# Performance work log

Hardware: AMD Instinct MI355X
Metric: run time of the kernel (lower is better)

## Reference

```python
import jax, jax.numpy as jnp
import numpy as np
from jax import lax

G, CPG, KS, N = 8, 8, 3, 9  # groups, channels per group, kernel size, ks*ks


def conv2d(x, w, b=None, pad=1):
    y = lax.conv_general_dilated(x, w, (1, 1), [(pad, pad), (pad, pad)],
                                 dimension_numbers=('NCHW', 'OIHW', 'NCHW'))
    if b is not None:
        y = y + b[None, :, None, None]
    return y


def deform_group(x, f, pw, pb, mw, mb, cw):
    # x: sampled feature (anchor slice), f: offset source (motion slice); both (b,c,h,w)
    b, c, h, w = x.shape
    offset = conv2d(f, pw, pb)                      # (b, 2N, h, w)
    m = jax.nn.sigmoid(conv2d(f, mw, mb))           # (b, N, h, w) modulation
    off = jnp.transpose(offset, (0, 2, 3, 1))       # (b, h, w, 2N): first N rows(x), last N cols(y)
    rng = jnp.arange(-1, 2, dtype=x.dtype)
    pn_x = jnp.repeat(rng, KS)                      # kernel row offset, n = kr*3 + kc
    pn_y = jnp.tile(rng, KS)                        # kernel col offset
    p0_x = jnp.arange(1, h + 1, dtype=x.dtype)[:, None, None]  # base grid starts at 1 (padding=0 here)
    p0_y = jnp.arange(1, w + 1, dtype=x.dtype)[None, :, None]
    px = p0_x + pn_x + off[..., :N]                 # (b, h, w, N)
    py = p0_y + pn_y + off[..., N:]
    fx = jnp.floor(lax.stop_gradient(px))           # p.detach().floor() in the original
    fy = jnp.floor(lax.stop_gradient(py))
    qx_lt = jnp.clip(fx, 0, h - 1)
    qx_rb = jnp.clip(fx + 1, 0, h - 1)
    qy_lt = jnp.clip(fy, 0, w - 1)
    qy_rb = jnp.clip(fy + 1, 0, w - 1)
    px = jnp.clip(px, 0, h - 1)
    py = jnp.clip(py, 0, w - 1)
    g_lt = (1 + (qx_lt - px)) * (1 + (qy_lt - py))
    g_rb = (1 - (qx_rb - px)) * (1 - (qy_rb - py))
    g_lb = (1 + (qx_lt - px)) * (1 - (qy_rb - py))
    g_rt = (1 - (qx_rb - px)) * (1 + (qy_lt - py))
    x_flat = x.reshape(b, c, h * w)

    def gather(ix, iy):
        idx = (ix * w + iy).astype(jnp.int32).reshape(b, 1, -1)  # (b,1,h*w*N)
        return jnp.take_along_axis(x_flat, idx, axis=2).reshape(b, c, h, w, N)

    x_off = (g_lt[:, None] * gather(qx_lt, qy_lt) + g_rb[:, None] * gather(qx_rb, qy_rb)
             + g_lb[:, None] * gather(qx_lt, qy_rb) + g_rt[:, None] * gather(qx_rb, qy_lt))
    x_off = x_off * jnp.transpose(m, (0, 2, 3, 1))[:, None]      # apply modulation mask
    # fused equivalent of reshape to (b,c,h*3,w*3) + conv(k=3, stride=3, no bias)
    return jnp.einsum('bchwn,ocn->bohw', x_off, cw.reshape(cw.shape[0], c, N))


def reference(o, anchor, pw, pb, mw, mb, cw, w1, b1, w2, b2):
    b, C, h, w = anchor.shape
    xg = anchor.reshape(b, G, CPG, h, w).transpose(1, 0, 2, 3, 4)  # (G,b,c,h,w)
    fg = o.reshape(b, G, CPG, h, w).transpose(1, 0, 2, 3, 4)
    tg = jax.vmap(deform_group)(xg, fg, pw, pb, mw, mb, cw)        # (G,b,c,h,w)
    target = tg.transpose(1, 0, 2, 3, 4).reshape(b, C, h, w)
    target_ = jnp.concatenate([target, anchor], axis=1)            # (b,128,h,w)
    return target + conv2d(conv2d(target_, w1, b1), w2, b2)


def setup_inputs() -> dict:
    key = jax.random.key(0)
    ks = jax.random.split(key, 11)
    B, C, H, W = 4, 64, 128, 128
    return {
        'o': jax.random.normal(ks[0], (B, C, H, W), jnp.float32),
        'anchor': jax.random.normal(ks[1], (B, C, H, W), jnp.float32),
        'pw': jax.random.normal(ks[2], (G, 2 * N, CPG, 3, 3), jnp.float32) * 0.05,
        'pb': jax.random.normal(ks[3], (G, 2 * N), jnp.float32) * 0.05,
        'mw': jax.random.normal(ks[4], (G, N, CPG, 3, 3), jnp.float32) * 0.05,
        'mb': jax.random.normal(ks[5], (G, N), jnp.float32) * 0.05,
        'cw': jax.random.normal(ks[6], (G, CPG, CPG, 3, 3), jnp.float32) * 0.05,
        'w1': jax.random.normal(ks[7], (64, 128, 3, 3), jnp.float32) * 0.05,
        'b1': jax.random.normal(ks[8], (64,), jnp.float32) * 0.05,
        'w2': jax.random.normal(ks[9], (64, 64, 3, 3), jnp.float32) * 0.05,
        'b2': jax.random.normal(ks[10], (64,), jnp.float32) * 0.05,
    }
```

## Files before the change

### kernel.cpp

```cpp
#include <hip/hip_runtime.h>


typedef __attribute__((ext_vector_type(8))) short short8;
typedef __attribute__((ext_vector_type(4))) float float4v;
typedef __attribute__((ext_vector_type(2))) float float2v;

#define MFMA_B16(a, b, c) __builtin_amdgcn_mfma_f32_16x16x32_bf16(a, b, c, 0, 0, 0)

__device__ __forceinline__ ushort f2bf(float f) {
    union { float f; unsigned u; } v; v.f = f;
    unsigned r = v.u + 0x7FFFu + ((v.u >> 16) & 1u);
    return (ushort)(r >> 16);
}
__device__ __forceinline__ float bf2f(ushort h) {
    union { unsigned u; float f; } v; v.u = ((unsigned)h) << 16;
    return v.f;
}

__device__ __forceinline__ void tap_wo(int gy, int gx, int n,
                                       float ox, float oy, float mzv,
                                       float* W, int* O)
{
    int ky = n / 3, kx = n - ky * 3;
    float pxf = (float)(gy + ky) + ox;
    float pyf = (float)(gx + kx) + oy;
    float fx = floorf(pxf), fy = floorf(pyf);
    float qxl = fminf(fmaxf(fx, 0.f), 127.f);
    float qxr = fminf(fmaxf(fx + 1.f, 0.f), 127.f);
    float qyl = fminf(fmaxf(fy, 0.f), 127.f);
    float qyr = fminf(fmaxf(fy + 1.f, 0.f), 127.f);
    float pxc = fminf(fmaxf(pxf, 0.f), 127.f);
    float pyc = fminf(fmaxf(pyf, 0.f), 127.f);
    float glx = 1.f + (qxl - pxc), grx = 1.f - (qxr - pxc);
    float gly = 1.f + (qyl - pyc), gry = 1.f - (qyr - pyc);
    float mm = 1.f / (1.f + __expf(-mzv));
    W[0] = glx * gly * mm; W[1] = grx * gry * mm;
    W[2] = glx * gry * mm; W[3] = grx * gly * mm;
    int ixl = (int)qxl, ixr = (int)qxr, iyl = (int)qyl, iyr = (int)qyr;
    O[0] = ixl * 128 + iyl; O[1] = ixr * 128 + iyr;
    O[2] = ixl * 128 + iyr; O[3] = ixr * 128 + iyl;
}

__device__ __forceinline__ short8 interp4(const float* W, const short8* cv)
{
    union U { short8 s; uint4 u; };
    uint4 c[4];
    #pragma unroll
    for (int j = 0; j < 4; ++j) { U t; t.s = cv[j]; c[j] = t.u; }
    U out;
    #pragma unroll
    for (int p = 0; p < 4; ++p) {
        float2v acc = {0.f, 0.f};
        #pragma unroll
        for (int j = 0; j < 4; ++j) {
            unsigned d = (&c[j].x)[p];
            float2v cc = {__uint_as_float(d << 16),
                          __uint_as_float(d & 0xffff0000u)};
            float2v Wv = {W[j], W[j]};
            acc = __builtin_elementwise_fma(cc, Wv, acc);
        }
        unsigned u0 = __float_as_uint(acc.x), u1 = __float_as_uint(acc.y);
        (&out.u.x)[p] = __builtin_amdgcn_perm(u1, u0, 0x07060302u);
    }
    return out.s;
}

__global__ __launch_bounds__(256) void prep(
    const float* __restrict__ anchor,
    const float* __restrict__ w1, const float* __restrict__ w2,
    const float* __restrict__ pw, const float* __restrict__ pb,
    const float* __restrict__ mw, const float* __restrict__ mb,
    const float* __restrict__ cw,
    ushort* __restrict__ anc_g,
    ushort* __restrict__ rw1, ushort* __restrict__ rw2,
    ushort* __restrict__ rpwh, ushort* __restrict__ rpwl,
    ushort* __restrict__ rcw)
{
    const int blk = blockIdx.x;
    if (blk < 256) {
        int pix = (blk & 63) * 256 + threadIdx.x;
        int b = blk >> 6;
        ushort tmp[64];
        #pragma unroll
        for (int ch = 0; ch < 64; ++ch)
            tmp[ch] = f2bf(anchor[(((size_t)(b * 64 + ch)) << 14) + pix]);
        #pragma unroll
        for (int grp = 0; grp < 8; ++grp) {
            short8 v;
            #pragma unroll
            for (int j = 0; j < 8; ++j) v[j] = (short)tmp[grp * 8 + j];
            *(short8*)(anc_g + ((size_t)(b * 8 + grp)) * 131072 + (size_t)pix * 8) = v;
        }
        return;
    }
    int i = (blk - 256) * 256 + threadIdx.x;
    if (i < 73728) {
        int kk = i & 31, r = i >> 5, oc = r & 63, r2 = r >> 6;
        int ks = r2 & 3, s = r2 >> 2, ic = ks * 32 + kk;
        rw1[i] = f2bf(w1[(oc * 128 + ic) * 9 + s]);
    }
    if (i < 36864) {
        int kk = i & 31, r = i >> 5, oc = r & 63, r2 = r >> 6;
        int ks = r2 & 1, s = r2 >> 1, ic = ks * 32 + kk;
        rw2[i] = f2bf(w2[(oc * 64 + ic) * 9 + s]);
    }
    if (i < 24576) {
        int kk = i & 31, r = i >> 5, n = r & 31, r2 = r >> 5;
        int ks = r2 % 3, g = r2 / 3, k = ks * 32 + kk;
        float v = 0.f;
        if (k < 72) {
            int s = k >> 3, ic = k & 7;
            if (n < 18)      v = pw[((g * 18 + n) * 8 + ic) * 9 + s];
            else if (n < 27) v = mw[((g * 9 + (n - 18)) * 8 + ic) * 9 + s];
        } else if (k == 72) {
            if (n < 18)      v = pb[g * 18 + n];
            else if (n < 27) v = mb[g * 9 + (n - 18)];
        }
        ushort h = f2bf(v);
        rpwh[i] = h;
        rpwl[i] = f2bf(v - bf2f(h));
    }
    if (i < 12288) {
        int kk = i & 31, r = i >> 5, oc = r & 15, r2 = r >> 4;
        int ks = r2 % 3, g = r2 / 3, k = ks * 32 + kk;
        float v = 0.f;
        if (k < 72 && oc < 8) {
            int n = k >> 3, ic = k & 7;
            v = cw[((g * 8 + oc) * 8 + ic) * 9 + n];
        }
        rcw[i] = f2bf(v);
    }
}

__global__ __launch_bounds__(256, 4) void deform_mfma(
    const float* __restrict__ o, const ushort* __restrict__ anc_g,
    const ushort* __restrict__ rpwh, const ushort* __restrict__ rpwl,
    const ushort* __restrict__ rcw,
    ushort* __restrict__ xcat_g)
{
    const int tile = blockIdx.x, g = blockIdx.y, b = blockIdx.z;
    const int ty0 = (tile >> 3) * 16, tx0 = (tile & 7) * 16;
    const int tid = threadIdx.x, lane = tid & 63, wave = tid >> 6;
    const int l15 = lane & 15, quad = lane >> 4;

    __shared__ __align__(16) ushort sU[19008];
    ushort* slabh = sU;
    ushort* slabl = sU + 2592;
    float*  sOff  = (float*)((char*)sU + 10368);
    ushort* sEu   = sU;

    const float* obase = o + (((size_t)(b * 64 + g * 8)) << 14);
    #pragma unroll
    for (int pass = 0; pass < 2; ++pass) {
        int pix = tid + pass * 256;
        if (pix < 324) {
            int r = pix / 18, c = pix - r * 18;
            int gy = ty0 + r - 1, gx = tx0 + c - 1;
            short8 vh = {0, 0, 0, 0, 0, 0, 0, 0};
            short8 vl = {0, 0, 0, 0, 0, 0, 0, 0};
            if ((unsigned)gy < 128u && (unsigned)gx < 128u) {
                const float* p0 = obase + (gy << 7) + gx;
                #pragma unroll
                for (int ic = 0; ic < 8; ++ic) {
                    float v = p0[(size_t)ic << 14];
                    ushort h = f2bf(v);
                    vh[ic] = (short)h;
                    vl[ic] = (short)f2bf(v - bf2f(h));
                }
            }
            *(short8*)(&slabh[pix * 8]) = vh;
            *(short8*)(&slabl[pix * 8]) = vl;
        }
    }
    __syncthreads();

    float4v offacc[4][2] = {};
    #pragma unroll
    for (int ks = 0; ks < 3; ++ks) {
        short8 Bh[2], Bl[2];
        #pragma unroll
        for (int nf = 0; nf < 2; ++nf) {
            int off = ((g * 3 + ks) * 32 + nf * 16 + l15) * 32 + quad * 8;
            Bh[nf] = *(const short8*)(rpwh + off);
            Bl[nf] = *(const short8*)(rpwl + off);
        }
        short8 Ah[4], Al[4];
        if (ks < 2) {
            int s = ks * 4 + quad, sy = s / 3, sx = s - sy * 3;
            #pragma unroll
            for (int py = 0; py < 4; ++py) {
                int row = wave * 4 + py;
                int sl = ((row + sy) * 18 + l15 + sx) * 8;
                Ah[py] = *(const short8*)(&slabh[sl]);
                Al[py] = *(const short8*)(&slabl[sl]);
            }
        } else {
            #pragma unroll
            for (int py = 0; py < 4; ++py) {
                short8 zh = {0, 0, 0, 0, 0, 0, 0, 0};
                short8 zl = {0, 0, 0, 0, 0, 0, 0, 0};
                if (quad == 0) {
                    int row = wave * 4 + py;
                    int sl = ((row + 2) * 18 + l15 + 2) * 8;
                    zh = *(const short8*)(&slabh[sl]);
                    zl = *(const short8*)(&slabl[sl]);
                } else if (quad == 1) {
                    zh[0] = (short)0x3F80;
                }
                Ah[py] = zh; Al[py] = zl;
            }
        }
        #pragma unroll
        for (int py = 0; py < 4; ++py)
            #pragma unroll
            for (int nf = 0; nf < 2; ++nf) {
                offacc[py][nf] = MFMA_B16(Ah[py], Bh[nf], offacc[py][nf]);
                offacc[py][nf] = MFMA_B16(Ah[py], Bl[nf], offacc[py][nf]);
                offacc[py][nf] = MFMA_B16(Al[py], Bh[nf], offacc[py][nf]);
            }
    }
    #pragma unroll
    for (int py = 0; py < 4; ++py) {
        int p0 = (wave * 4 + py) * 16 + quad * 4;
        #pragma unroll
        for (int nf = 0; nf < 2; ++nf) {
            int ch = nf * 16 + l15;
            if (ch < 27) {
                #pragma unroll
                for (int reg = 0; reg < 4; ++reg)
                    sOff[(p0 + reg) * 27 + ch] = offacc[py][nf][reg];
            }
        }
    }

    short8 Bw[3];
    #pragma unroll
    for (int ks = 0; ks < 3; ++ks)
        Bw[ks] = *(const short8*)(rcw + (((g * 3 + ks) * 16 + l15) * 32 + quad * 8));

    const ushort* gb = anc_g + ((size_t)(b * 8 + g)) * 131072;
    const int n1 = quad, n2 = quad + 4;
    float4v cacc[4] = {};
    #pragma unroll
    for (int py = 0; py < 4; ++py) {
        int prow = wave * 4 + py;
        int p = prow * 16 + l15;
        int gy = ty0 + prow, gx = tx0 + l15;

        float W[8]; int O[8];
        tap_wo(gy, gx, n1, sOff[p * 27 + n1], sOff[p * 27 + 9 + n1],
               sOff[p * 27 + 18 + n1], &W[0], &O[0]);
        tap_wo(gy, gx, n2, sOff[p * 27 + n2], sOff[p * 27 + 9 + n2],
               sOff[p * 27 + 18 + n2], &W[4], &O[4]);
        short8 cv[8];
        #pragma unroll
        for (int j = 0; j < 8; ++j)
            cv[j] = *(const short8*)(gb + (size_t)O[j] * 8);
        short8 A0 = interp4(&W[0], &cv[0]);
        short8 A1 = interp4(&W[4], &cv[4]);
        short8 A2 = {0, 0, 0, 0, 0, 0, 0, 0};
        if (quad == 0) {
            float W2[4]; int O2[4];
            tap_wo(gy, gx, 8, sOff[p * 27 + 8], sOff[p * 27 + 17],
                   sOff[p * 27 + 26], W2, O2);
            short8 c2[4];
            #pragma unroll
            for (int j = 0; j < 4; ++j)
                c2[j] = *(const short8*)(gb + (size_t)O2[j] * 8);
            A2 = interp4(W2, c2);
        }
        cacc[py] = MFMA_B16(A0, Bw[0], cacc[py]);
        cacc[py] = MFMA_B16(A1, Bw[1], cacc[py]);
        cacc[py] = MFMA_B16(A2, Bw[2], cacc[py]);
    }

    __syncthreads();
    #pragma unroll
    for (int py = 0; py < 4; ++py) {
        if (l15 < 8) {
            #pragma unroll
            for (int reg = 0; reg < 4; ++reg)
                sEu[((wave * 4 + py) * 16 + quad * 4 + reg) * 8 + l15] =
                    f2bf(cacc[py][reg]);
        }
    }
    __syncthreads();
    {
        const int gy = ty0 + (tid >> 4), gx = tx0 + (tid & 15);
        short8 pk = *(const short8*)(&sEu[tid * 8]);
        *(short8*)(xcat_g + ((size_t)(b * 8 + g)) * 131072
                   + (size_t)((gy << 7) + gx) * 8) = pk;
    }
}

__global__ __launch_bounds__(256, 4) void conv1_mfma(
    const ushort* __restrict__ xg, const ushort* __restrict__ ag,
    const ushort* __restrict__ rw1, const float* __restrict__ b1,
    ushort* __restrict__ t1)
{
    const int patch = blockIdx.x, b = blockIdx.y;
    const int px0 = (patch & 7) * 16, py0 = (patch >> 3) * 8;
    const int tid = threadIdx.x, lane = tid & 63, wave = tid >> 6;
    const int mhalf = wave & 1, nhalf = wave >> 1;
    const int l15 = lane & 15, quad = lane >> 4;

    __shared__ __align__(16) ushort sA[180 * 72];

    float4v acc[4][2] = {};
    #pragma unroll
    for (int ph = 0; ph < 2; ++ph) {
        if (ph) __syncthreads();
        const ushort* src = (ph == 0) ? xg : ag;
        for (int task = tid; task < 1440; task += 256) {
            int grp = task / 180, pix = task - grp * 180;
            int r = pix / 18, c = pix - r * 18;
            int gy = py0 + r - 1, gx = px0 + c - 1;
            short8 v = {0, 0, 0, 0, 0, 0, 0, 0};
            if ((unsigned)gy < 128u && (unsigned)gx < 128u) {
                const ushort* plane = src + ((size_t)(b * 8 + grp)) * 131072;
                v = *(const short8*)(plane + (size_t)((gy << 7) + gx) * 8);
            }
            *(short8*)(&sA[pix * 72 + grp * 8]) = v;
        }
        __syncthreads();

        #pragma unroll
        for (int ks2 = 0; ks2 < 2; ++ks2) {
            const int ks = ph * 2 + ks2;
            #pragma unroll
            for (int ky = 0; ky < 3; ++ky) {
                short8 Bf[3][2];
                #pragma unroll
                for (int kx = 0; kx < 3; ++kx)
                    #pragma unroll
                    for (int nf = 0; nf < 2; ++nf) {
                        int oc = nhalf * 32 + nf * 16 + l15;
                        Bf[kx][nf] = *(const short8*)(rw1 +
                            ((((ky * 3 + kx) * 4 + ks) * 64 + oc) * 32 + quad * 8));
                    }
                #pragma unroll
                for (int py = 0; py < 4; ++py) {
                    int slabrow = mhalf * 4 + py + ky;
                    #pragma unroll
                    for (int kx = 0; kx < 3; ++kx) {
                        short8 A = *(const short8*)(&sA[(slabrow * 18 + l15 + kx) * 72
                                                        + ks2 * 32 + quad * 8]);
                        #pragma unroll
                        for (int nf = 0; nf < 2; ++nf)
                            acc[py][nf] = MFMA_B16(A, Bf[kx][nf], acc[py][nf]);
                    }
                }
            }
        }
    }
    __syncthreads();
    ushort* sE = sA;
    #pragma unroll
    for (int nf = 0; nf < 2; ++nf) {
        int oc = nhalf * 32 + nf * 16 + l15;
        float bias = b1[oc];
        #pragma unroll
        for (int py = 0; py < 4; ++py) {
            int row = mhalf * 4 + py;
            #pragma unroll
            for (int reg = 0; reg < 4; ++reg)
                sE[(row * 16 + quad * 4 + reg) * 64 + oc] = f2bf(acc[py][nf][reg] + bias);
        }
    }
    __syncthreads();
    {
        const size_t nbase = ((size_t)b) << 20;
        int pix = tid >> 1, half = tid & 1;
        int gy = py0 + (pix >> 4), gx = px0 + (pix & 15);
        ushort* dst = t1 + nbase + (size_t)((gy << 7) + gx) * 64 + half * 32;
        const ushort* sp = sE + pix * 64 + half * 32;
        #pragma unroll
        for (int j = 0; j < 4; ++j)
            *(short8*)(dst + j * 8) = *(const short8*)(sp + j * 8);
    }
}

__global__ __launch_bounds__(256, 4) void conv2_mfma(
    const ushort* __restrict__ t1, const ushort* __restrict__ rw2,
    const float* __restrict__ b2, const ushort* __restrict__ xg,
    float* __restrict__ out)
{
    const int patch = blockIdx.x, b = blockIdx.y;
    const int px0 = (patch & 7) * 16, py0 = (patch >> 3) * 8;
    const int tid = threadIdx.x, lane = tid & 63, wave = tid >> 6;
    const int ohalf = wave & 1, rhalf = wave >> 1;
    const int l15 = lane & 15, quad = lane >> 4;

    __shared__ __align__(16) ushort sX[180 * 72];

    const size_t nbase = ((size_t)b) << 20;
    for (int task = tid; task < 1440; task += 256) {
        int pix = task >> 3, grp = task & 7;
        int r = pix / 18, c = pix - r * 18;
        int gy = py0 + r - 1, gx = px0 + c - 1;
        short8 v = {0, 0, 0, 0, 0, 0, 0, 0};
        if ((unsigned)gy < 128u && (unsigned)gx < 128u)
            v = *(const short8*)(t1 + nbase + (size_t)((gy << 7) + gx) * 64 + grp * 8);
        *(short8*)(&sX[pix * 72 + grp * 8]) = v;
    }
    __syncthreads();

    float4v acc[2][4] = {};
    #pragma unroll
    for (int ks = 0; ks < 2; ++ks) {
        #pragma unroll
        for (int ky = 0; ky < 3; ++ky) {
            short8 Aw[3][2];
            #pragma unroll
            for (int kx = 0; kx < 3; ++kx)
                #pragma unroll
                for (int mf = 0; mf < 2; ++mf) {
                    int oc = ohalf * 32 + mf * 16 + l15;
                    Aw[kx][mf] = *(const short8*)(rw2 +
                        ((((ky * 3 + kx) * 2 + ks) * 64 + oc) * 32 + quad * 8));
                }
            #pragma unroll
            for (int py = 0; py < 4; ++py) {
                int slabrow = rhalf * 4 + py + ky;
                #pragma unroll
                for (int kx = 0; kx < 3; ++kx) {
                    short8 Bx = *(const short8*)(&sX[(slabrow * 18 + l15 + kx) * 72
                                                     + ks * 32 + quad * 8]);
                    #pragma unroll
                    for (int mf = 0; mf < 2; ++mf)
                        acc[mf][py] = MFMA_B16(Aw[kx][mf], Bx, acc[mf][py]);
                }
            }
        }
    }
    #pragma unroll
    for (int mf = 0; mf < 2; ++mf)
        #pragma unroll
        for (int reg = 0; reg < 4; ++reg) {
            int oc = ohalf * 32 + mf * 16 + quad * 4 + reg;
            float bias = b2[oc];
            const ushort* rplane = xg + ((size_t)(b * 8 + (oc >> 3))) * 131072 + (oc & 7);
            #pragma unroll
            for (int py = 0; py < 4; ++py) {
                int gy = py0 + rhalf * 4 + py, gx = px0 + l15;
                int pix = (gy << 7) + gx;
                float res = bf2f(rplane[(size_t)pix * 8]);
                out[(((size_t)(b * 64 + oc)) << 14) + pix] = acc[mf][py][reg] + bias + res;
            }
        }
}

extern "C" void kernel_launch(void* const* d_in, const int* in_sizes, int n_in,
                              void* d_out, int out_size, void* d_ws, size_t ws_size,
                              hipStream_t stream) {
    const float* o      = (const float*)d_in[0];
    const float* anchor = (const float*)d_in[1];
    const float* pw     = (const float*)d_in[2];
    const float* pb     = (const float*)d_in[3];
    const float* mw     = (const float*)d_in[4];
    const float* mb     = (const float*)d_in[5];
    const float* cw     = (const float*)d_in[6];
    const float* w1     = (const float*)d_in[7];
    const float* b1     = (const float*)d_in[8];
    const float* w2     = (const float*)d_in[9];
    const float* b2     = (const float*)d_in[10];
    float* out = (float*)d_out;

    char* ws = (char*)d_ws;
    ushort* anc_g  = (ushort*)(ws);
    ushort* xcat_g = (ushort*)(ws + 8388608);
    ushort* t1b    = (ushort*)(ws + 16777216);
    char*   wsm    = ws + 25165824;
    ushort* rw1p   = (ushort*)(wsm);
    ushort* rw2p   = (ushort*)(wsm + 147456);
    ushort* rpwh   = (ushort*)(wsm + 147456 + 73728);
    ushort* rpwl   = (ushort*)(wsm + 147456 + 73728 + 49152);
    ushort* rcwp   = (ushort*)(wsm + 147456 + 73728 + 98304);

    prep<<<544, 256, 0, stream>>>(anchor, w1, w2, pw, pb, mw, mb, cw,
                                  anc_g, rw1p, rw2p, rpwh, rpwl, rcwp);
    deform_mfma<<<dim3(64, 8, 4), 256, 0, stream>>>(o, anc_g, rpwh, rpwl, rcwp,
                                                    xcat_g);
    conv1_mfma<<<dim3(128, 4), 256, 0, stream>>>(xcat_g, anc_g, rw1p, b1, t1b);
    conv2_mfma<<<dim3(128, 4), 256, 0, stream>>>(t1b, rw2p, b2, xcat_g, out);
}
```

Measured before the change: 164.9 us.

## Fuse conv1 and conv2 into one kernel with halo recompute in LDS

Merges the two 3x3 conv kernels into one. Each block computes conv1 over an 18x10 halo region (padded up to 192 pixels) from a 20x12 input slab and keeps the bf16 intermediate in shared memory, then runs conv2 from it. This drops the global write and read of the t1 intermediate and one kernel launch. In exchange it recomputes conv1 on halo pixels (about 1.5x the conv1 MFMA work), doubles the per-wave conv1 accumulators, and lowers the launch-bounds occupancy target from 4 to 2 blocks per CU.

Result: no change. 164.1 us (-0.5%).

```diff
diff --git a/kernel.cpp b/kernel.cpp
--- a/kernel.cpp
+++ b/kernel.cpp
@@ -293,161 +293,118 @@
     }
 }
 
-__global__ __launch_bounds__(256, 4) void conv1_mfma(
+__global__ __launch_bounds__(256, 2) void conv12_mfma(
     const ushort* __restrict__ xg, const ushort* __restrict__ ag,
     const ushort* __restrict__ rw1, const float* __restrict__ b1,
-    ushort* __restrict__ t1)
-{
-    const int patch = blockIdx.x, b = blockIdx.y;
-    const int px0 = (patch & 7) * 16, py0 = (patch >> 3) * 8;
-    const int tid = threadIdx.x, lane = tid & 63, wave = tid >> 6;
-    const int mhalf = wave & 1, nhalf = wave >> 1;
-    const int l15 = lane & 15, quad = lane >> 4;
-
-    __shared__ __align__(16) ushort sA[180 * 72];
-
-    float4v acc[4][2] = {};
-    #pragma unroll
-    for (int ph = 0; ph < 2; ++ph) {
-        if (ph) __syncthreads();
-        const ushort* src = (ph == 0) ? xg : ag;
-        for (int task = tid; task < 1440; task += 256) {
-            int grp = task / 180, pix = task - grp * 180;
-            int r = pix / 18, c = pix - r * 18;
-            int gy = py0 + r - 1, gx = px0 + c - 1;
-            short8 v = {0, 0, 0, 0, 0, 0, 0, 0};
-            if ((unsigned)gy < 128u && (unsigned)gx < 128u) {
-                const ushort* plane = src + ((size_t)(b * 8 + grp)) * 131072;
-                v = *(const short8*)(plane + (size_t)((gy << 7) + gx) * 8);
-            }
-            *(short8*)(&sA[pix * 72 + grp * 8]) = v;
-        }
-        __syncthreads();
-
-        #pragma unroll
-        for (int ks2 = 0; ks2 < 2; ++ks2) {
-            const int ks = ph * 2 + ks2;
-            #pragma unroll
-            for (int ky = 0; ky < 3; ++ky) {
-                short8 Bf[3][2];
-                #pragma unroll
-                for (int kx = 0; kx < 3; ++kx)
-                    #pragma unroll
-                    for (int nf = 0; nf < 2; ++nf) {
-                        int oc = nhalf * 32 + nf * 16 + l15;
-                        Bf[kx][nf] = *(const short8*)(rw1 +
-                            ((((ky * 3 + kx) * 4 + ks) * 64 + oc) * 32 + quad * 8));
-                    }
-                #pragma unroll
-                for (int py = 0; py < 4; ++py) {
-                    int slabrow = mhalf * 4 + py + ky;
-                    #pragma unroll
-                    for (int kx = 0; kx < 3; ++kx) {
-                        short8 A = *(const short8*)(&sA[(slabrow * 18 + l15 + kx) * 72
-                                                        + ks2 * 32 + quad * 8]);
-                        #pragma unroll
-                        for (int nf = 0; nf < 2; ++nf)
-                            acc[py][nf] = MFMA_B16(A, Bf[kx][nf], acc[py][nf]);
-                    }
-                }
-            }
-        }
-    }
-    __syncthreads();
-    ushort* sE = sA;
-    #pragma unroll
-    for (int nf = 0; nf < 2; ++nf) {
-        int oc = nhalf * 32 + nf * 16 + l15;
-        float bias = b1[oc];
-        #pragma unroll
-        for (int py = 0; py < 4; ++py) {
-            int row = mhalf * 4 + py;
-            #pragma unroll
-            for (int reg = 0; reg < 4; ++reg)
-                sE[(row * 16 + quad * 4 + reg) * 64 + oc] = f2bf(acc[py][nf][reg] + bias);
-        }
-    }
-    __syncthreads();
-    {
-        const size_t nbase = ((size_t)b) << 20;
-        int pix = tid >> 1, half = tid & 1;
-        int gy = py0 + (pix >> 4), gx = px0 + (pix & 15);
-        ushort* dst = t1 + nbase + (size_t)((gy << 7) + gx) * 64 + half * 32;
-        const ushort* sp = sE + pix * 64 + half * 32;
-        #pragma unroll
-        for (int j = 0; j < 4; ++j)
-            *(short8*)(dst + j * 8) = *(const short8*)(sp + j * 8);
-    }
-}
-
-__global__ __launch_bounds__(256, 4) void conv2_mfma(
-    const ushort* __restrict__ t1, const ushort* __restrict__ rw2,
-    const float* __restrict__ b2, const ushort* __restrict__ xg,
+    const ushort* __restrict__ rw2, const float* __restrict__ b2,
     float* __restrict__ out)
 {
     const int patch = blockIdx.x, b = blockIdx.y;
     const int px0 = (patch & 7) * 16, py0 = (patch >> 3) * 8;
     const int tid = threadIdx.x, lane = tid & 63, wave = tid >> 6;
-    const int ohalf = wave & 1, rhalf = wave >> 1;
     const int l15 = lane & 15, quad = lane >> 4;
 
-    __shared__ __align__(16) ushort sX[180 * 72];
-
-    const size_t nbase = ((size_t)b) << 20;
-    for (int task = tid; task < 1440; task += 256) {
-        int pix = task >> 3, grp = task & 7;
-        int r = pix / 18, c = pix - r * 18;
-        int gy = py0 + r - 1, gx = px0 + c - 1;
-        short8 v = {0, 0, 0, 0, 0, 0, 0, 0};
-        if ((unsigned)gy < 128u && (unsigned)gx < 128u)
-            v = *(const short8*)(t1 + nbase + (size_t)((gy << 7) + gx) * 64 + grp * 8);
-        *(short8*)(&sX[pix * 72 + grp * 8]) = v;
+    __shared__ __align__(16) ushort sA[240 * 72];
+
+    int base[3];
+    #pragma unroll
+    for (int j = 0; j < 3; ++j) {
+        int q = 48 * wave + 16 * j + l15;
+        int qe = q < 180 ? q : 179;
+        int r = qe / 18, c = qe - r * 18;
+        base[j] = r * 20 + c;
+    }
+
+    float4v acc1[3][4] = {};
+    #pragma unroll
+    for (int ph = 0; ph < 2; ++ph) {
+        if (ph) __syncthreads();
+        const ushort* src = (ph == 0) ? xg : ag;
+        if (tid < 240) {
+            int ri = tid / 20, ci = tid - ri * 20;
+            int gy = py0 - 2 + ri, gx = px0 - 2 + ci;
+            bool in = ((unsigned)gy < 128u) && ((unsigned)gx < 128u);
+            size_t poff = (size_t)((gy << 7) + gx) * 8;
+            #pragma unroll
+            for (int grp = 0; grp < 8; ++grp) {
+                short8 v = {0, 0, 0, 0, 0, 0, 0, 0};
+                if (in)
+                    v = *(const short8*)(src + ((size_t)(b * 8 + grp)) * 131072 + poff);
+                *(short8*)(&sA[tid * 72 + grp * 8]) = v;
+            }
+        }
+        __syncthreads();
+
+        #pragma unroll
+        for (int ks2 = 0; ks2 < 2; ++ks2) {
+            const int ks = ph * 2 + ks2;
+            #pragma unroll
+            for (int s = 0; s < 9; ++s) {
+                const int ky = s / 3, kx = s - ky * 3;
+                short8 Bf[4];
+                #pragma unroll
+                for (int nf = 0; nf < 4; ++nf)
+                    Bf[nf] = *(const short8*)(rw1 +
+                        (((s * 4 + ks) * 64 + nf * 16 + l15) * 32 + quad * 8));
+                #pragma unroll
+                for (int j = 0; j < 3; ++j) {
+                    short8 A = *(const short8*)(&sA[(base[j] + ky * 20 + kx) * 72
+                                                    + ks2 * 32 + quad * 8]);
+                    #pragma unroll
+                    for (int nf = 0; nf < 4; ++nf)
+                        acc1[j][nf] = MFMA_B16(A, Bf[nf], acc1[j][nf]);
+                }
+            }
+        }
     }
     __syncthreads();
-
-    float4v acc[2][4] = {};
+    ushort* sT1 = sA;
+    #pragma unroll
+    for (int j = 0; j < 3; ++j) {
+        #pragma unroll
+        for (int reg = 0; reg < 4; ++reg) {
+            int q = 48 * wave + 16 * j + quad * 4 + reg;
+            int r = q / 18, c = q - r * 18;
+            int gy = py0 - 1 + r, gx = px0 - 1 + c;
+            bool in = ((unsigned)gy < 128u) && ((unsigned)gx < 128u);
+            #pragma unroll
+            for (int nf = 0; nf < 4; ++nf) {
+                int oc = nf * 16 + l15;
+                float v = acc1[j][nf][reg] + b1[oc];
+                sT1[q * 72 + oc] = in ? f2bf(v) : (ushort)0;
+            }
+        }
+    }
+    __syncthreads();
+
+    float4v acc2[8] = {};
     #pragma unroll
     for (int ks = 0; ks < 2; ++ks) {
         #pragma unroll
-        for (int ky = 0; ky < 3; ++ky) {
-            short8 Aw[3][2];
-            #pragma unroll
-            for (int kx = 0; kx < 3; ++kx)
-                #pragma unroll
-                for (int mf = 0; mf < 2; ++mf) {
-                    int oc = ohalf * 32 + mf * 16 + l15;
-                    Aw[kx][mf] = *(const short8*)(rw2 +
-                        ((((ky * 3 + kx) * 2 + ks) * 64 + oc) * 32 + quad * 8));
-                }
-            #pragma unroll
-            for (int py = 0; py < 4; ++py) {
-                int slabrow = rhalf * 4 + py + ky;
-                #pragma unroll
-                for (int kx = 0; kx < 3; ++kx) {
-                    short8 Bx = *(const short8*)(&sX[(slabrow * 18 + l15 + kx) * 72
-                                                     + ks * 32 + quad * 8]);
-                    #pragma unroll
-                    for (int mf = 0; mf < 2; ++mf)
-                        acc[mf][py] = MFMA_B16(Aw[kx][mf], Bx, acc[mf][py]);
-                }
-            }
-        }
-    }
-    #pragma unroll
-    for (int mf = 0; mf < 2; ++mf)
+        for (int s = 0; s < 9; ++s) {
+            const int ky = s / 3, kx = s - ky * 3;
+            short8 Aw = *(const short8*)(rw2 +
+                (((s * 2 + ks) * 64 + wave * 16 + l15) * 32 + quad * 8));
+            #pragma unroll
+            for (int f = 0; f < 8; ++f) {
+                int q = (f + ky) * 18 + l15 + kx;
+                short8 Bx = *(const short8*)(&sT1[q * 72 + ks * 32 + quad * 8]);
+                acc2[f] = MFMA_B16(Aw, Bx, acc2[f]);
+            }
+        }
+    }
+    #pragma unroll
+    for (int f = 0; f < 8; ++f) {
+        int gy = py0 + f, gx = px0 + l15;
+        int pix = (gy << 7) + gx;
         #pragma unroll
         for (int reg = 0; reg < 4; ++reg) {
-            int oc = ohalf * 32 + mf * 16 + quad * 4 + reg;
-            float bias = b2[oc];
-            const ushort* rplane = xg + ((size_t)(b * 8 + (oc >> 3))) * 131072 + (oc & 7);
-            #pragma unroll
-            for (int py = 0; py < 4; ++py) {
-                int gy = py0 + rhalf * 4 + py, gx = px0 + l15;
-                int pix = (gy << 7) + gx;
-                float res = bf2f(rplane[(size_t)pix * 8]);
-                out[(((size_t)(b * 64 + oc)) << 14) + pix] = acc[mf][py][reg] + bias + res;
-            }
-        }
+            int oc = wave * 16 + quad * 4 + reg;
+            float res = bf2f(xg[((size_t)(b * 8 + (oc >> 3))) * 131072
+                               + (size_t)pix * 8 + (oc & 7)]);
+            out[(((size_t)(b * 64 + oc)) << 14) + pix] = acc2[f][reg] + b2[oc] + res;
+        }
+    }
 }
 
 extern "C" void kernel_launch(void* const* d_in, const int* in_sizes, int n_in,
@@ -469,8 +426,7 @@
     char* ws = (char*)d_ws;
     ushort* anc_g  = (ushort*)(ws);
     ushort* xcat_g = (ushort*)(ws + 8388608);
-    ushort* t1b    = (ushort*)(ws + 16777216);
-    char*   wsm    = ws + 25165824;
+    char*   wsm    = ws + 16777216;
     ushort* rw1p   = (ushort*)(wsm);
     ushort* rw2p   = (ushort*)(wsm + 147456);
     ushort* rpwh   = (ushort*)(wsm + 147456 + 73728);
@@ -481,6 +437,6 @@
                                   anc_g, rw1p, rw2p, rpwh, rpwl, rcwp);
     deform_mfma<<<dim3(64, 8, 4), 256, 0, stream>>>(o, anc_g, rpwh, rpwl, rcwp,
                                                     xcat_g);
-    conv1_mfma<<<dim3(128, 4), 256, 0, stream>>>(xcat_g, anc_g, rw1p, b1, t1b);
-    conv2_mfma<<<dim3(128, 4), 256, 0, stream>>>(t1b, rw2p, b2, xcat_g, out);
-}
+    conv12_mfma<<<dim3(128, 4), 256, 0, stream>>>(xcat_g, anc_g, rw1p, b1,
+                                                  rw2p, b2, out);
+}
```
